# Kernel optimization log

Hardware: AMD Instinct MI355X
Metric: run time of the kernel (lower is better)

The kernel has to match this reference:

```python
import jax, jax.numpy as jnp
import numpy as np
from jax import lax

K = 3
STRIDE = 1
PAD = 1


def _active_sites(mask):
    # mask: [B, Cm, H, W] int. A patch is 'active' if ANY element of the
    # unfolded (im2col) patch is nonzero -> max-pool of (mask != 0) over the
    # same kernel/stride/padding window.
    m = jnp.any(mask != 0, axis=1, keepdims=True).astype(jnp.float32)  # [B,1,H,W]
    pooled = lax.reduce_window(
        m, 0.0, lax.max,
        window_dimensions=(1, 1, K, K),
        window_strides=(1, 1, STRIDE, STRIDE),
        padding=((0, 0), (0, 0), (PAD, PAD), (PAD, PAD)))
    return pooled > 0  # [B,1,H_out,W_out] bool


def reference(x, mask, weight, bias):
    # Faithful math of MyConv: conv2d(x, weight) + bias at active patch sites
    # (patches whose mask window contains any nonzero), exact zeros elsewhere.
    # masked_scatter in the original preserves patch order, so this equals
    # active * (conv + bias).
    conv = lax.conv_general_dilated(
        x, weight,
        window_strides=(STRIDE, STRIDE),
        padding=((PAD, PAD), (PAD, PAD)),
        dimension_numbers=('NCHW', 'OIHW', 'NCHW'))  # [B,C_out,H_out,W_out]
    active = _active_sites(mask)
    out = (conv + bias[None, :, None, None]) * active.astype(conv.dtype)
    return out


def setup_inputs() -> dict:
    key = jax.random.key(0)
    k1, k2, k3, k4 = jax.random.split(key, 4)
    B, C_in, C_out, H, W = 8, 128, 128, 128, 128
    x = jax.random.normal(k1, (B, C_in, H, W), dtype=jnp.float32)
    mask = jax.random.randint(k2, (B, 1, H, W), 0, 2, dtype=jnp.int32)
    fan_in = C_in * K * K
    bound = 1.0 / np.sqrt(fan_in)
    weight = jax.random.uniform(k3, (C_out, C_in, K, K), minval=-bound, maxval=bound, dtype=jnp.float32)
    bias = jax.random.uniform(k4, (C_out,), minval=-bound, maxval=bound, dtype=jnp.float32)
    return {"x": x, "mask": mask, "weight": weight, "bias": bias}
```

## Files before the change

### kernel.cpp

```cpp
#include <hip/hip_runtime.h>


typedef __bf16 bf16x8 __attribute__((ext_vector_type(8)));
typedef unsigned short u16x8 __attribute__((ext_vector_type(8)));
typedef float f32x4 __attribute__((ext_vector_type(4)));

__device__ __forceinline__ unsigned short f2bf(float f) {
    unsigned int u = __float_as_uint(f);
    u += 0x7fffu + ((u >> 16) & 1u);
    return (unsigned short)(u >> 16);
}

__global__ void cvt_x3(const float* __restrict__ x, unsigned short* __restrict__ xp) {
    __shared__ float Lf[32 * 132];
    const int t   = threadIdx.x;
    const int hh2 = blockIdx.x % 130;
    const int cb  = (blockIdx.x / 130) & 3;
    const int b   = blockIdx.x / 520;
    u16x8* slab = (u16x8*)(xp + (size_t)(((b * 4 + cb) * 130 + hh2)) * 4160);
    const u16x8 z = {0, 0, 0, 0, 0, 0, 0, 0};

    if (hh2 == 0 || hh2 == 129) {
        for (int k = t; k < 520; k += 256) slab[k] = z;
        return;
    }
    const int h = hh2 - 1;

    #pragma unroll
    for (int u = 0; u < 4; ++u) {
        const int f  = t + 256 * u;
        const int ci = f >> 5;
        const int w4 = f & 31;
        const float4 v = *(const float4*)(x + (((b * 128 + cb * 32 + ci) * 128 + h) << 7) + (w4 << 2));
        *(float4*)&Lf[ci * 132 + (w4 << 2)] = v;
    }
    __syncthreads();

    for (int k = t; k < 520; k += 256) {
        const int r = k >> 2;
        const int c = k & 3;
        u16x8 o;
        if (r == 0 || r == 129) {
            o = z;
        } else {
            const int w   = r - 1;
            const int ci0 = (c ^ (r & 3)) << 3;
            #pragma unroll
            for (int s = 0; s < 8; ++s) o[s] = f2bf(Lf[(ci0 + s) * 132 + w]);
        }
        slab[k] = o;
    }
}

__global__ void pack_w2(const float* __restrict__ wgt, unsigned short* __restrict__ wp) {
    const int e    = blockIdx.x * 256 + threadIdx.x;
    const int j    = e & 31;
    const int m    = (e >> 5) & 127;
    const int r    = e >> 12;
    const int kw   = r - (r / 3) * 3;
    const int cbkh = r / 3;
    const int cb   = cbkh & 3;
    const int kh   = cbkh >> 2;
    const int ci   = cb * 32 + j;
    wp[e] = f2bf(wgt[((m * 128 + ci) * 3 + kh) * 3 + kw]);
}

__global__ __launch_bounds__(256, 2)
void myconv4(const unsigned short* __restrict__ xp,
             const int* __restrict__ mask,
             const unsigned short* __restrict__ wp,
             const float* __restrict__ bias,
             float* __restrict__ out)
{
    __shared__ unsigned char Xs[16640];
    __shared__ float act[256];

    const int t  = threadIdx.x;
    const int b  = blockIdx.x >> 6;
    const int h0 = (blockIdx.x & 63) << 1;

    {
        const int g = t >> 7;
        const int w = t & 127;
        const int h = h0 + g;
        int any = 0;
        #pragma unroll
        for (int kh = 0; kh < 3; ++kh) {
            int hh = h + kh - 1;
            if ((unsigned)hh < 128u) {
                const int* mrow = mask + (b * 128 + hh) * 128;
                #pragma unroll
                for (int kw = 0; kw < 3; ++kw) {
                    int ww = w + kw - 1;
                    if ((unsigned)ww < 128u) any |= mrow[ww];
                }
            }
        }
        act[t] = any ? 1.0f : 0.0f;
    }

    const int lane = t & 63;
    const int l16  = lane & 15;
    const int q    = lane >> 4;
    const int wv   = t >> 6;
    const int wm   = (wv & 1) << 6;
    const int g    = wv >> 1;

    f32x4 acc[4][8];
    const f32x4 fzero = {0.f, 0.f, 0.f, 0.f};
    #pragma unroll
    for (int i = 0; i < 4; ++i)
        #pragma unroll
        for (int j = 0; j < 8; ++j)
            acc[i][j] = fzero;

    int bb[3];
    #pragma unroll
    for (int kw = 0; kw < 3; ++kw)
        bb[kw] = g * 8320 + (l16 + kw) * 64 + ((q ^ ((l16 + kw) & 3)) << 4);

    const unsigned char* agl = (const unsigned char*)wp + (wm + l16) * 64 + q * 16;
    const unsigned char* xpB = (const unsigned char*)xp;

    for (int kh = 0; kh < 3; ++kh) {
        for (int cb = 0; cb < 4; ++cb) {
            __syncthreads();

            const unsigned char* gx =
                xpB + (size_t)((b * 4 + cb) * 130 + h0 + kh) * 8320;
            #pragma unroll
            for (int u = 0; u < 4; ++u)
                __builtin_amdgcn_global_load_lds(
                    (const __attribute__((address_space(1))) unsigned int*)(gx + ((wv << 2) + u) * 1024 + lane * 16),
                    (__attribute__((address_space(3))) unsigned int*)(Xs + ((wv << 2) + u) * 1024),
                    16, 0, 0);
            if (t < 16)
                __builtin_amdgcn_global_load_lds(
                    (const __attribute__((address_space(1))) unsigned int*)(gx + 16384 + t * 16),
                    (__attribute__((address_space(3))) unsigned int*)(Xs + 16384),
                    16, 0, 0);

            __syncthreads();

            const unsigned char* ar = agl + (kh * 4 + cb) * 24576;
            #pragma unroll
            for (int kw = 0; kw < 3; ++kw) {
                bf16x8 af[4];
                #pragma unroll
                for (int i = 0; i < 4; ++i)
                    af[i] = *(const bf16x8*)(ar + kw * 8192 + i * 1024);
                bf16x8 bfr[8];
                #pragma unroll
                for (int j = 0; j < 8; ++j)
                    bfr[j] = *(const bf16x8*)(Xs + bb[kw] + j * 1024);
                #pragma unroll
                for (int i = 0; i < 4; ++i)
                    #pragma unroll
                    for (int j = 0; j < 8; ++j)
                        acc[i][j] = __builtin_amdgcn_mfma_f32_16x16x32_bf16(af[i], bfr[j], acc[i][j], 0, 0, 0);
            }
        }
    }

    #pragma unroll
    for (int i = 0; i < 4; ++i) {
        const f32x4 bv = *(const f32x4*)(bias + wm + (i << 4) + (q << 2));
        #pragma unroll
        for (int j = 0; j < 8; ++j) {
            const int w = (j << 4) + l16;
            const float a = act[(g << 7) + w];
            float* base = out + (((((b << 7) + wm + (i << 4) + (q << 2)) << 7) + h0 + g) << 7) + w;
            #pragma unroll
            for (int rg = 0; rg < 4; ++rg)
                base[rg << 14] = (acc[i][j][rg] + bv[rg]) * a;
        }
    }
}

#define LDAF 40
__global__ __launch_bounds__(256, 2)
void myconv_fb(const float* __restrict__ x,
               const int* __restrict__ mask,
               const float* __restrict__ wgt,
               const float* __restrict__ bias,
               float* __restrict__ out)
{
    __shared__ unsigned short As[128 * LDAF];
    __shared__ unsigned short Bs[128 * LDAF];
    __shared__ float act[128];

    const int t   = threadIdx.x;
    const int blk = blockIdx.x;
    const int b   = blk >> 7;
    const int h   = blk & 127;

    if (t < 128) {
        int any = 0;
        #pragma unroll
        for (int kh = 0; kh < 3; ++kh) {
            int hh = h + kh - 1;
            if ((unsigned)hh < 128u) {
                const int* mrow = mask + (b * 128 + hh) * 128;
                #pragma unroll
                for (int kw = 0; kw < 3; ++kw) {
                    int ww = t + kw - 1;
                    if ((unsigned)ww < 128u) any |= mrow[ww];
                }
            }
        }
        act[t] = any ? 1.0f : 0.0f;
    }

    const int lane = t & 63;
    const int l16  = lane & 15;
    const int half = lane >> 4;
    const int wv   = t >> 6;
    const int wm   = (wv >> 1) << 6;
    const int wn   = (wv & 1) << 6;

    f32x4 acc[4][4];
    const f32x4 fzero = {0.f, 0.f, 0.f, 0.f};
    #pragma unroll
    for (int i = 0; i < 4; ++i)
        #pragma unroll
        for (int j = 0; j < 4; ++j)
            acc[i][j] = fzero;

    const int am  = t >> 3;
    const int ac4 = (t & 7) << 2;
    const int n     = t & 127;
    const int khalf = __builtin_amdgcn_readfirstlane(t >> 7);
    const int xb    = b << 21;

    for (int kt = 0; kt < 36; ++kt) {
        __syncthreads();
        #pragma unroll
        for (int jj = 0; jj < 4; ++jj) {
            const int m = am + (jj << 5);
            const float4 v = *(const float4*)(wgt + m * 1152 + kt * 32 + ac4);
            unsigned short* dst = &As[m * LDAF + ac4];
            dst[0] = f2bf(v.x); dst[1] = f2bf(v.y); dst[2] = f2bf(v.z); dst[3] = f2bf(v.w);
        }
        u16x8 bv0, bv1;
        #pragma unroll
        for (int s = 0; s < 16; ++s) {
            const int k  = kt * 32 + khalf * 16 + s;
            const int ci = (k * 7282) >> 16;
            const int r  = k - ci * 9;
            const int kh = (r >= 3) + (r >= 6);
            const int kw = r - kh * 3;
            const int hh = h + kh - 1;
            float v = 0.f;
            if ((unsigned)hh < 128u) {
                const int ww = n + kw - 1;
                if ((unsigned)ww < 128u)
                    v = x[xb + (ci << 14) + (hh << 7) + ww];
            }
            if (s < 8) bv0[s] = f2bf(v); else bv1[s - 8] = f2bf(v);
        }
        *(u16x8*)&Bs[n * LDAF + khalf * 16]     = bv0;
        *(u16x8*)&Bs[n * LDAF + khalf * 16 + 8] = bv1;

        __syncthreads();

        bf16x8 af[4], bfr[4];
        #pragma unroll
        for (int i = 0; i < 4; ++i)
            af[i] = *(const bf16x8*)&As[(wm + (i << 4) + l16) * LDAF + (half << 3)];
        #pragma unroll
        for (int j = 0; j < 4; ++j)
            bfr[j] = *(const bf16x8*)&Bs[(wn + (j << 4) + l16) * LDAF + (half << 3)];
        #pragma unroll
        for (int i = 0; i < 4; ++i)
            #pragma unroll
            for (int j = 0; j < 4; ++j)
                acc[i][j] = __builtin_amdgcn_mfma_f32_16x16x32_bf16(af[i], bfr[j], acc[i][j], 0, 0, 0);
    }

    #pragma unroll
    for (int i = 0; i < 4; ++i) {
        #pragma unroll
        for (int j = 0; j < 4; ++j) {
            const int ncol = wn + (j << 4) + l16;
            const float a  = act[ncol];
            #pragma unroll
            for (int rg = 0; rg < 4; ++rg) {
                const int m = wm + (i << 4) + (half << 2) + rg;
                out[(((b << 7) + m) << 14) + (h << 7) + ncol] =
                    (acc[i][j][rg] + bias[m]) * a;
            }
        }
    }
}

extern "C" void kernel_launch(void* const* d_in, const int* in_sizes, int n_in,
                              void* d_out, int out_size, void* d_ws, size_t ws_size,
                              hipStream_t stream) {
    const float* x    = (const float*)d_in[0];
    const int*   mask = (const int*)d_in[1];
    const float* wgt  = (const float*)d_in[2];
    const float* bias = (const float*)d_in[3];
    float* out        = (float*)d_out;

    const size_t XP_ELEMS = 4160ull * 4160;
    const size_t WP_ELEMS = 36ull * 128 * 32;
    const size_t need = (XP_ELEMS + WP_ELEMS) * 2;

    if (ws_size >= need) {
        unsigned short* xpw = (unsigned short*)d_ws;
        unsigned short* wpw = xpw + XP_ELEMS;
        cvt_x3<<<dim3(4160), dim3(256), 0, stream>>>(x, xpw);
        pack_w2<<<dim3(576), dim3(256), 0, stream>>>(wgt, wpw);
        myconv4<<<dim3(512), dim3(256), 0, stream>>>(xpw, mask, wpw, bias, out);
    } else {
        myconv_fb<<<dim3(1024), dim3(256), 0, stream>>>(x, mask, wgt, bias, out);
    }
}
```

Measured before the change: 155.3 us.

## Double-buffer LDS slabs, split output channels across blocks, merge prep kernels

The conv kernel now uses a two-slab LDS double buffer, so the global-to-LDS load for the next (kh, cb) step is issued before the MFMA work on the current one. Each block drops to 128 threads and handles one half of the output channels, giving twice as many blocks. The LDS swizzle changes to (r + r>>2)&3 to reduce bank conflicts, and the x-conversion and weight-packing kernels are merged into one launch. In exchange, the input slabs are now read twice (once per channel half), LDS use per block roughly doubles, and the single barrier per step relies on correct ordering of the async loads.

```diff
diff --git a/kernel.cpp b/kernel.cpp
--- a/kernel.cpp
+++ b/kernel.cpp
@@ -11,12 +11,28 @@
     return (unsigned short)(u >> 16);
 }
 
-__global__ void cvt_x3(const float* __restrict__ x, unsigned short* __restrict__ xp) {
+__global__ void setup_all(const float* __restrict__ x, const float* __restrict__ wgt,
+                          unsigned short* __restrict__ xp, unsigned short* __restrict__ wpp) {
     __shared__ float Lf[32 * 132];
     const int t   = threadIdx.x;
-    const int hh2 = blockIdx.x % 130;
-    const int cb  = (blockIdx.x / 130) & 3;
-    const int b   = blockIdx.x / 520;
+    const int bid = blockIdx.x;
+
+    if (bid >= 4160) {
+        const int e    = (bid - 4160) * 256 + t;
+        const int j    = e & 31;
+        const int m    = (e >> 5) & 127;
+        const int r    = e >> 12;
+        const int kw   = r - (r / 3) * 3;
+        const int cbkh = r / 3;
+        const int cb   = cbkh & 3;
+        const int kh   = cbkh >> 2;
+        wpp[e] = f2bf(wgt[((m * 128 + cb * 32 + j) * 3 + kh) * 3 + kw]);
+        return;
+    }
+
+    const int hh2 = bid % 130;
+    const int cb  = (bid / 130) & 3;
+    const int b   = bid / 520;
     u16x8* slab = (u16x8*)(xp + (size_t)(((b * 4 + cb) * 130 + hh2)) * 4160);
     const u16x8 z = {0, 0, 0, 0, 0, 0, 0, 0};
 
@@ -44,7 +60,7 @@
             o = z;
         } else {
             const int w   = r - 1;
-            const int ci0 = (c ^ (r & 3)) << 3;
+            const int ci0 = (c ^ ((r + (r >> 2)) & 3)) << 3;
             #pragma unroll
             for (int s = 0; s < 8; ++s) o[s] = f2bf(Lf[(ci0 + s) * 132 + w]);
         }
@@ -52,37 +68,49 @@
     }
 }
 
-__global__ void pack_w2(const float* __restrict__ wgt, unsigned short* __restrict__ wp) {
-    const int e    = blockIdx.x * 256 + threadIdx.x;
-    const int j    = e & 31;
-    const int m    = (e >> 5) & 127;
-    const int r    = e >> 12;
-    const int kw   = r - (r / 3) * 3;
-    const int cbkh = r / 3;
-    const int cb   = cbkh & 3;
-    const int kh   = cbkh >> 2;
-    const int ci   = cb * 32 + j;
-    wp[e] = f2bf(wgt[((m * 128 + ci) * 3 + kh) * 3 + kw]);
-}
-
-__global__ __launch_bounds__(256, 2)
-void myconv4(const unsigned short* __restrict__ xp,
+__device__ __forceinline__ void stage_slabs(const unsigned char* gx, unsigned char* ls, int t) {
+    const int g    = t >> 6;
+    const int lane = t & 63;
+    #pragma unroll
+    for (int u = 0; u < 8; ++u)
+        __builtin_amdgcn_global_load_lds(
+            (const __attribute__((address_space(1))) unsigned int*)(gx + u * 2048 + g * 1024 + lane * 16),
+            (__attribute__((address_space(3))) unsigned int*)(ls + u * 2048 + g * 1024),
+            16, 0, 0);
+    if (t < 16)
+        __builtin_amdgcn_global_load_lds(
+            (const __attribute__((address_space(1))) unsigned int*)(gx + 16384 + t * 16),
+            (__attribute__((address_space(3))) unsigned int*)(ls + 16384),
+            16, 0, 0);
+}
+
+__global__ __launch_bounds__(128, 2)
+void myconv5(const unsigned short* __restrict__ xp,
              const int* __restrict__ mask,
              const unsigned short* __restrict__ wp,
              const float* __restrict__ bias,
              float* __restrict__ out)
 {
-    __shared__ unsigned char Xs[16640];
+    __shared__ __align__(16) unsigned char Xs[2][16640];
     __shared__ float act[256];
 
-    const int t  = threadIdx.x;
-    const int b  = blockIdx.x >> 6;
-    const int h0 = (blockIdx.x & 63) << 1;
-
-    {
-        const int g = t >> 7;
-        const int w = t & 127;
-        const int h = h0 + g;
+    const int t     = threadIdx.x;
+    const int b     = blockIdx.x >> 7;
+    const int mhalf = (blockIdx.x >> 6) & 1;
+    const int h0    = (blockIdx.x & 63) << 1;
+
+    const int lane = t & 63;
+    const int l16  = lane & 15;
+    const int q    = lane >> 4;
+    const int g    = t >> 6;
+
+    const unsigned char* xpB = (const unsigned char*)xp;
+
+    stage_slabs(xpB + (size_t)((b * 4 + 0) * 130 + h0 + 0) * 8320, &Xs[0][0], t);
+
+    #pragma unroll
+    for (int gg = 0; gg < 2; ++gg) {
+        const int h = h0 + gg;
         int any = 0;
         #pragma unroll
         for (int kh = 0; kh < 3; ++kh) {
@@ -91,20 +119,23 @@
                 const int* mrow = mask + (b * 128 + hh) * 128;
                 #pragma unroll
                 for (int kw = 0; kw < 3; ++kw) {
-                    int ww = w + kw - 1;
+                    int ww = t + kw - 1;
                     if ((unsigned)ww < 128u) any |= mrow[ww];
                 }
             }
         }
-        act[t] = any ? 1.0f : 0.0f;
-    }
-
-    const int lane = t & 63;
-    const int l16  = lane & 15;
-    const int q    = lane >> 4;
-    const int wv   = t >> 6;
-    const int wm   = (wv & 1) << 6;
-    const int g    = wv >> 1;
+        act[gg * 128 + t] = any ? 1.0f : 0.0f;
+    }
+
+    int bb[3];
+    #pragma unroll
+    for (int kw = 0; kw < 3; ++kw) {
+        const int rr   = l16 + kw;
+        const int slot = q ^ ((rr + (rr >> 2)) & 3);
+        bb[kw] = g * 8320 + rr * 64 + (slot << 4);
+    }
+
+    const unsigned char* agl = (const unsigned char*)wp + (mhalf * 64 + l16) * 64 + q * 16;
 
     f32x4 acc[4][8];
     const f32x4 fzero = {0.f, 0.f, 0.f, 0.f};
@@ -114,62 +145,46 @@
         for (int j = 0; j < 8; ++j)
             acc[i][j] = fzero;
 
-    int bb[3];
-    #pragma unroll
-    for (int kw = 0; kw < 3; ++kw)
-        bb[kw] = g * 8320 + (l16 + kw) * 64 + ((q ^ ((l16 + kw) & 3)) << 4);
-
-    const unsigned char* agl = (const unsigned char*)wp + (wm + l16) * 64 + q * 16;
-    const unsigned char* xpB = (const unsigned char*)xp;
-
-    for (int kh = 0; kh < 3; ++kh) {
-        for (int cb = 0; cb < 4; ++cb) {
-            __syncthreads();
-
-            const unsigned char* gx =
-                xpB + (size_t)((b * 4 + cb) * 130 + h0 + kh) * 8320;
-            #pragma unroll
-            for (int u = 0; u < 4; ++u)
-                __builtin_amdgcn_global_load_lds(
-                    (const __attribute__((address_space(1))) unsigned int*)(gx + ((wv << 2) + u) * 1024 + lane * 16),
-                    (__attribute__((address_space(3))) unsigned int*)(Xs + ((wv << 2) + u) * 1024),
-                    16, 0, 0);
-            if (t < 16)
-                __builtin_amdgcn_global_load_lds(
-                    (const __attribute__((address_space(1))) unsigned int*)(gx + 16384 + t * 16),
-                    (__attribute__((address_space(3))) unsigned int*)(Xs + 16384),
-                    16, 0, 0);
-
-            __syncthreads();
-
-            const unsigned char* ar = agl + (kh * 4 + cb) * 24576;
-            #pragma unroll
-            for (int kw = 0; kw < 3; ++kw) {
-                bf16x8 af[4];
-                #pragma unroll
-                for (int i = 0; i < 4; ++i)
-                    af[i] = *(const bf16x8*)(ar + kw * 8192 + i * 1024);
-                bf16x8 bfr[8];
+    __syncthreads();
+
+    for (int r = 0; r < 12; ++r) {
+        if (r < 11) {
+            const int rn = r + 1;
+            stage_slabs(xpB + (size_t)((b * 4 + (rn & 3)) * 130 + h0 + (rn >> 2)) * 8320,
+                        &Xs[(rn & 1)][0], t);
+        }
+
+        const unsigned char* ar = agl + r * 24576;
+        const unsigned char* xb = &Xs[r & 1][0];
+        #pragma unroll
+        for (int kw = 0; kw < 3; ++kw) {
+            bf16x8 af[4];
+            #pragma unroll
+            for (int i = 0; i < 4; ++i)
+                af[i] = *(const bf16x8*)(ar + kw * 8192 + i * 1024);
+            bf16x8 bfr[8];
+            #pragma unroll
+            for (int j = 0; j < 8; ++j)
+                bfr[j] = *(const bf16x8*)(xb + bb[kw] + j * 1024);
+            #pragma unroll
+            for (int i = 0; i < 4; ++i)
                 #pragma unroll
                 for (int j = 0; j < 8; ++j)
-                    bfr[j] = *(const bf16x8*)(Xs + bb[kw] + j * 1024);
-                #pragma unroll
-                for (int i = 0; i < 4; ++i)
-                    #pragma unroll
-                    for (int j = 0; j < 8; ++j)
-                        acc[i][j] = __builtin_amdgcn_mfma_f32_16x16x32_bf16(af[i], bfr[j], acc[i][j], 0, 0, 0);
-            }
-        }
+                    acc[i][j] = __builtin_amdgcn_mfma_f32_16x16x32_bf16(af[i], bfr[j], acc[i][j], 0, 0, 0);
+        }
+
+        __syncthreads();
     }
 
     #pragma unroll
     for (int i = 0; i < 4; ++i) {
-        const f32x4 bv = *(const f32x4*)(bias + wm + (i << 4) + (q << 2));
+        const int m0 = mhalf * 64 + (i << 4) + (q << 2);
+        const f32x4 bv = *(const f32x4*)(bias + m0);
         #pragma unroll
         for (int j = 0; j < 8; ++j) {
             const int w = (j << 4) + l16;
             const float a = act[(g << 7) + w];
-            float* base = out + (((((b << 7) + wm + (i << 4) + (q << 2)) << 7) + h0 + g) << 7) + w;
+            float* base = out + (((b << 7) + m0) << 14) + ((h0 + g) << 7) + w;
             #pragma unroll
             for (int rg = 0; rg < 4; ++rg)
                 base[rg << 14] = (acc[i][j][rg] + bv[rg]) * a;
@@ -309,9 +324,8 @@
     if (ws_size >= need) {
         unsigned short* xpw = (unsigned short*)d_ws;
         unsigned short* wpw = xpw + XP_ELEMS;
-        cvt_x3<<<dim3(4160), dim3(256), 0, stream>>>(x, xpw);
-        pack_w2<<<dim3(576), dim3(256), 0, stream>>>(wgt, wpw);
-        myconv4<<<dim3(512), dim3(256), 0, stream>>>(xpw, mask, wpw, bias, out);
+        setup_all<<<dim3(4736), dim3(256), 0, stream>>>(x, wgt, xpw, wpw);
+        myconv5<<<dim3(1024), dim3(128), 0, stream>>>(xpw, mask, wpw, bias, out);
     } else {
         myconv_fb<<<dim3(1024), dim3(256), 0, stream>>>(x, mask, wgt, bias, out);
     }
```

After: 150.9 us. 2.8% less time.
